# Optimization experiments

Measured on AMD Instinct MI355X. Metric: run time of the kernel, lower is better.

The kernel has to match this reference:

```python
import jax, jax.numpy as jnp
import numpy as np

H, KV, D, HID = 36, 4, 128, 4608   # heads, kv heads, head_dim, hidden
THETA = 100000.0
NEG = -1e30


def _rope_neox(pos, x):
    # pos: [T] int, x: [T, nh, D]; neox style: rotate half
    half = D // 2
    inv_freq = 1.0 / (THETA ** (jnp.arange(half, dtype=jnp.float32) / half))
    ang = pos.astype(jnp.float32)[:, None] * inv_freq          # [T, half]
    cos = jnp.cos(ang)[:, None, :]
    sin = jnp.sin(ang)[:, None, :]
    x1, x2 = x[..., :half], x[..., half:]
    return jnp.concatenate([x1 * cos - x2 * sin, x2 * cos + x1 * sin], axis=-1)


def setup_inputs() -> dict:
    key = jax.random.key(0)
    ks = jax.random.split(key, 6)
    T = 2048
    return {
        "positions": jnp.arange(T, dtype=jnp.int32),
        "hidden_states": jax.random.normal(ks[0], (T, HID), dtype=jnp.float32),
        "wqkv": jax.random.normal(ks[1], (H * D + 2 * KV * D, HID), dtype=jnp.float32) * 0.02,
        "bqkv": jax.random.normal(ks[2], (H * D + 2 * KV * D,), dtype=jnp.float32) * 0.02,
        "wo": jax.random.normal(ks[3], (HID, H * D), dtype=jnp.float32) * 0.02,
        "bo": jax.random.normal(ks[4], (HID,), dtype=jnp.float32) * 0.02,
        "window": 1024,
    }


def reference(positions, hidden_states, wqkv, bqkv, wo, bo, window):
    T = hidden_states.shape[0]
    qkv = hidden_states @ wqkv.T + bqkv                         # [T, 5632]
    q, k, v = jnp.split(qkv, [H * D, H * D + KV * D], axis=-1)
    q = q.reshape(T, H, D)
    k = k.reshape(T, KV, D)
    v = v.reshape(T, KV, D)
    q = _rope_neox(positions, q)
    k = _rope_neox(positions, k)
    # GQA: expand kv heads to query heads
    g = H // KV
    k = jnp.repeat(k, g, axis=1)                                # [T, H, D]
    v = jnp.repeat(v, g, axis=1)
    scale = D ** -0.5
    scores = jnp.einsum('thd,shd->hts', q, k) * scale           # [H, T, T]
    t = jnp.arange(T)
    # causal + sliding window: attend to s in (t - window, t]
    mask = (t[None, :] <= t[:, None]) & (t[None, :] > t[:, None] - window)
    scores = jnp.where(mask[None, :, :], scores, NEG)
    p = jax.nn.softmax(scores, axis=-1)
    attn = jnp.einsum('hts,shd->thd', p, v).reshape(T, H * D)
    return attn @ wo.T + bo
```

## Files before the change

kernel.cpp:

```cpp
#include <hip/hip_runtime.h>
#include <hip/hip_bf16.h>
#include <math.h>


#define T_SEQ   2048
#define HIDDEN  4608
#define NHEAD   36
#define NKVH    4
#define HEADDIM 128
#define GQA_G   9
#define NQKV    5632
#define KOFF    4608
#define VOFF    5120
#define BQ 64
#define BS 32
#define NTILE   64
#define PSTR 40

typedef short    bf16x8 __attribute__((ext_vector_type(8)));
typedef _Float16 f16x8  __attribute__((ext_vector_type(8)));
typedef _Float16 f16x4  __attribute__((ext_vector_type(4)));
typedef float    f32x4  __attribute__((ext_vector_type(4)));

__device__ inline bf16x8 pack8(float4 u, float4 v) {
    union { bf16x8 v8; __hip_bfloat162 h[4]; } r;
    r.h[0] = __float22bfloat162_rn(make_float2(u.x, u.y));
    r.h[1] = __float22bfloat162_rn(make_float2(u.z, u.w));
    r.h[2] = __float22bfloat162_rn(make_float2(v.x, v.y));
    r.h[3] = __float22bfloat162_rn(make_float2(v.z, v.w));
    return r.v8;
}

typedef const __attribute__((address_space(1))) int* gas_ptr;
typedef __attribute__((address_space(3))) int*       las_ptr;
__device__ __forceinline__ void gload_lds16(const void* g, void* l) {
    __builtin_amdgcn_global_load_lds((gas_ptr)g, (las_ptr)l, 16, 0, 0);
}

__global__ __launch_bounds__(256)
void cvt_bf16_kernel(const float* __restrict__ in, __hip_bfloat16* __restrict__ out,
                     int n8)
{
    for (int i = blockIdx.x * 256 + threadIdx.x; i < n8; i += gridDim.x * 256) {
        const float4 a = *(const float4*)(in + (size_t)i * 8);
        const float4 b = *(const float4*)(in + (size_t)i * 8 + 4);
        *(bf16x8*)(out + (size_t)i * 8) = pack8(a, b);
    }
}

template <typename OutT>
__global__ __launch_bounds__(256)
void gemm_bf16bt_kernel(const __hip_bfloat16* __restrict__ A,
                        const __hip_bfloat16* __restrict__ B,
                        const float* __restrict__ bias,
                        OutT* __restrict__ C, int N, int K)
{
    __shared__ short As[2][128 * 32];
    __shared__ short Bs[2][128 * 32];

    const int tid  = threadIdx.x;
    const int lane = tid & 63;
    const int wave = tid >> 6;

    const int nbx = gridDim.x;
    const int nwg = nbx * gridDim.y;
    int lin = blockIdx.y * nbx + blockIdx.x;
    lin = (lin & 7) * (nwg >> 3) + (lin >> 3);
    const int row0 = (lin / nbx) * 128;
    const int col0 = (lin % nbx) * 128;

    const int wr   = (wave >> 1) * 64;
    const int wc   = (wave & 1) * 64;
    const int fr   = lane & 15;
    const int fk   = (lane >> 4) * 8;

    const int srow = lane >> 2;
    const int scol = (lane & 3) * 8;

    const __hip_bfloat16* Ag0 = A + (size_t)(row0 + wave * 32 + srow) * K + scol;
    const __hip_bfloat16* Ag1 = Ag0 + (size_t)16 * K;
    const __hip_bfloat16* Bg0 = B + (size_t)(col0 + wave * 32 + srow) * K + scol;
    const __hip_bfloat16* Bg1 = Bg0 + (size_t)16 * K;

    short* Al0[2] = { &As[0][(wave * 32) * 32],      &As[1][(wave * 32) * 32] };
    short* Al1[2] = { &As[0][(wave * 32 + 16) * 32], &As[1][(wave * 32 + 16) * 32] };
    short* Bl0[2] = { &Bs[0][(wave * 32) * 32],      &Bs[1][(wave * 32) * 32] };
    short* Bl1[2] = { &Bs[0][(wave * 32 + 16) * 32], &Bs[1][(wave * 32 + 16) * 32] };

    f32x4 acc[4][4];
    #pragma unroll
    for (int i = 0; i < 4; ++i)
        #pragma unroll
        for (int j = 0; j < 4; ++j)
            #pragma unroll
            for (int r = 0; r < 4; ++r) acc[i][j][r] = 0.0f;

    gload_lds16(Ag0, Al0[0]);
    gload_lds16(Ag1, Al1[0]);
    gload_lds16(Bg0, Bl0[0]);
    gload_lds16(Bg1, Bl1[0]);
    __syncthreads();
    int cur = 0;

    for (int k0 = 0; k0 < K; k0 += 32) {
        if (k0 + 32 < K) {
            const int kn = k0 + 32;
            const int nb = cur ^ 1;
            gload_lds16(Ag0 + kn, Al0[nb]);
            gload_lds16(Ag1 + kn, Al1[nb]);
            gload_lds16(Bg0 + kn, Bl0[nb]);
            gload_lds16(Bg1 + kn, Bl1[nb]);
        }

        bf16x8 af[4], bfr[4];
        #pragma unroll
        for (int i = 0; i < 4; ++i)
            af[i] = *(const bf16x8*)&As[cur][(wr + i * 16 + fr) * 32 + fk];
        #pragma unroll
        for (int j = 0; j < 4; ++j)
            bfr[j] = *(const bf16x8*)&Bs[cur][(wc + j * 16 + fr) * 32 + fk];

        #pragma unroll
        for (int i = 0; i < 4; ++i)
            #pragma unroll
            for (int j = 0; j < 4; ++j)
                acc[i][j] = __builtin_amdgcn_mfma_f32_16x16x32_bf16(
                    af[i], bfr[j], acc[i][j], 0, 0, 0);

        __syncthreads();
        cur ^= 1;
    }

    const int quad = lane >> 4;
    #pragma unroll
    for (int j = 0; j < 4; ++j) {
        const int col = col0 + wc + j * 16 + fr;
        const float bv = bias[col];
        #pragma unroll
        for (int i = 0; i < 4; ++i) {
            const int rowb = row0 + wr + i * 16 + quad * 4;
            #pragma unroll
            for (int r = 0; r < 4; ++r)
                C[(size_t)(rowb + r) * N + col] = (OutT)(acc[i][j][r] + bv);
        }
    }
}

__global__ __launch_bounds__(256)
void prep_kv_kernel(const int* __restrict__ positions,
                    const _Float16* __restrict__ qkv,
                    _Float16* __restrict__ Kt,
                    _Float16* __restrict__ Vt)
{
    const int tile = blockIdx.x;
    const int kvh  = blockIdx.y;
    const int t    = threadIdx.x;
    const size_t ib = ((size_t)kvh * NTILE + tile) * 4096;

    {
        const int s   = t >> 3;
        const int j8  = (t & 7) * 8;
        const int row = tile * BS + s;
        const _Float16* kp = qkv + (size_t)row * NQKV + KOFF + kvh * HEADDIM;
        const f16x8 xa = *(const f16x8*)(kp + j8);
        const f16x8 xb = *(const f16x8*)(kp + 64 + j8);
        const float pos = (float)positions[row];
        f16x8 H1, H2;
        #pragma unroll
        for (int j = 0; j < 8; ++j) {
            const int d = j8 + j;
            const float inv_freq = __expf(-(float)d * (11.512925465f / 64.0f));
            float sn, cs;
            sincosf(pos * inv_freq, &sn, &cs);
            const float x1 = (float)xa[j];
            const float x2 = (float)xb[j];
            H1[j] = (_Float16)(x1 * cs - x2 * sn);
            H2[j] = (_Float16)(x2 * cs + x1 * sn);
        }
        const int gd1 = (t & 7);
        const int gd2 = gd1 + 8;
        *(f16x8*)&Kt[ib + gd1 * 256 + s * 8] = H1;
        *(f16x8*)&Kt[ib + gd2 * 256 + s * 8] = H2;
    }

    {
        const int q  = t >> 6;
        const int d0 = (t & 63) * 2;
        const _Float16* vp = qkv + (size_t)(tile * BS + q * 8) * NQKV + VOFF
                           + kvh * HEADDIM + d0;
        f16x8 V0, V1;
        #pragma unroll
        for (int j = 0; j < 8; ++j) {
            union { unsigned u; _Float16 h[2]; } w;
            w.u = *(const unsigned*)(vp + (size_t)j * NQKV);
            V0[j] = w.h[0];
            V1[j] = w.h[1];
        }
        *(f16x8*)&Vt[ib + q * 1024 + d0 * 8]       = V0;
        *(f16x8*)&Vt[ib + q * 1024 + (d0 + 1) * 8] = V1;
    }
}

__global__ __launch_bounds__(256)
void attn_kernel(const _Float16* __restrict__ qkv,
                 const int* __restrict__ positions,
                 const _Float16* __restrict__ Kt,
                 const _Float16* __restrict__ Vt,
                 __hip_bfloat16* __restrict__ out,
                 const int* __restrict__ windowp)
{
    __shared__ _Float16 KS[2][4096];
    __shared__ _Float16 VS[2][4096];
    __shared__ _Float16 Ps[4][16 * PSTR];

    const int h    = blockIdx.x;
    const int q0   = (T_SEQ / BQ - 1 - blockIdx.y) * BQ;
    const int kvh  = h / GQA_G;
    const int tid  = threadIdx.x;
    const int lane = tid & 63;
    const int wave = tid >> 6;
    const int l15  = lane & 15;
    const int quad = lane >> 4;
    const int window = *windowp;
    const float scale = 0.088388347648318447f * 1.4426950408889634f;

    f16x8 qf[4];
    const int q_g = q0 + wave * 16 + l15;
    {
        const _Float16* qp = qkv + (size_t)q_g * NQKV + h * HEADDIM + quad * 8;
        float qv[32];
        #pragma unroll
        for (int ks = 0; ks < 4; ++ks) {
            const f16x8 qa = *(const f16x8*)(qp + ks * 32);
            #pragma unroll
            for (int j = 0; j < 8; ++j) qv[ks * 8 + j] = (float)qa[j];
        }
        const float pos = (float)positions[q_g];
        #pragma unroll
        for (int p = 0; p < 2; ++p)
            #pragma unroll
            for (int j = 0; j < 8; ++j) {
                const int d = p * 32 + quad * 8 + j;
                const float inv_freq = __expf(-(float)d * (11.512925465f / 64.0f));
                float sn, cs;
                sincosf(pos * inv_freq, &sn, &cs);
                const float x1 = qv[p * 8 + j];
                const float x2 = qv[(p + 2) * 8 + j];
                qv[p * 8 + j]       = x1 * cs - x2 * sn;
                qv[(p + 2) * 8 + j] = x2 * cs + x1 * sn;
            }
        #pragma unroll
        for (int ks = 0; ks < 4; ++ks)
            #pragma unroll
            for (int j = 0; j < 8; ++j)
                qf[ks][j] = (_Float16)(qv[ks * 8 + j] * scale);
    }

    f32x4 o[8];
    #pragma unroll
    for (int c = 0; c < 8; ++c)
        #pragma unroll
        for (int r = 0; r < 4; ++r) o[c][r] = 0.0f;
    float mrun = -1e9f;
    float lrun = 0.0f;

    int s_lo = q0 - window + 1;
    if (s_lo < 0) s_lo = 0;
    s_lo &= ~(BS - 1);
    const int tile0  = s_lo >> 5;
    const int ntiles = ((q0 + BQ) - s_lo) >> 5;

    const _Float16* gK = Kt + ((size_t)kvh * NTILE) * 4096;
    const _Float16* gV = Vt + ((size_t)kvh * NTILE) * 4096;

    _Float16* Psw = &Ps[wave][0];

    auto STAGE = [&](int buf, int tile) {
        const size_t toff = (size_t)tile * 4096;
        #pragma unroll
        for (int i = 0; i < 2; ++i) {
            const int off = (wave * 2 + i) * 512;
            gload_lds16(gK + toff + off + lane * 8, &KS[buf][off]);
            gload_lds16(gV + toff + off + lane * 8, &VS[buf][off]);
        }
    };

    STAGE(0, tile0);
    __syncthreads();
    int cur = 0;

    for (int it = 0; it < ntiles; ++it) {
        const int st = s_lo + it * BS;
        if (it + 1 < ntiles) STAGE(cur ^ 1, tile0 + it + 1);

        f32x4 acc0, acc1;
        #pragma unroll
        for (int r = 0; r < 4; ++r) { acc0[r] = 0.0f; acc1[r] = 0.0f; }
        #pragma unroll
        for (int ks = 0; ks < 4; ++ks) {
            const int g = (ks * 4 + quad) * 256;
            const f16x8 b0 = *(const f16x8*)&KS[cur][g + l15 * 8];
            const f16x8 b1 = *(const f16x8*)&KS[cur][g + (16 + l15) * 8];
            acc0 = __builtin_amdgcn_mfma_f32_16x16x32_f16(b0, qf[ks], acc0, 0, 0, 0);
            acc1 = __builtin_amdgcn_mfma_f32_16x16x32_f16(b1, qf[ks], acc1, 0, 0, 0);
        }

        const int dq = q_g - st;
        float sv[8];
        #pragma unroll
        for (int r = 0; r < 4; ++r) {
            const int o0 = quad * 4 + r;
            const bool v0 = (unsigned)(dq - o0)      < (unsigned)window;
            const bool v1 = (unsigned)(dq - o0 - 16) < (unsigned)window;
            sv[r]     = v0 ? acc0[r] : -2e9f;
            sv[4 + r] = v1 ? acc1[r] : -2e9f;
        }
        float mx = sv[0];
        #pragma unroll
        for (int i = 1; i < 8; ++i) mx = fmaxf(mx, sv[i]);
        mx = fmaxf(mx, __shfl_xor(mx, 16));
        mx = fmaxf(mx, __shfl_xor(mx, 32));
        if (__any(mx > mrun + 8.0f)) {
            const float mnew  = fmaxf(mrun, mx);
            const float alpha = __builtin_amdgcn_exp2f(mrun - mnew);
            mrun = mnew;
            lrun *= alpha;
            #pragma unroll
            for (int c = 0; c < 8; ++c)
                #pragma unroll
                for (int r = 0; r < 4; ++r) o[c][r] *= alpha;
        }
        float e[8];
        float sum = 0.0f;
        #pragma unroll
        for (int i = 0; i < 8; ++i) {
            e[i] = __builtin_amdgcn_exp2f(sv[i] - mrun);
            sum += e[i];
        }
        sum += __shfl_xor(sum, 16);
        sum += __shfl_xor(sum, 32);
        lrun += sum;

        f16x4 pl, ph;
        #pragma unroll
        for (int r = 0; r < 4; ++r) { pl[r] = (_Float16)e[r]; ph[r] = (_Float16)e[4 + r]; }
        *(f16x4*)&Psw[l15 * PSTR + quad * 4]      = pl;
        *(f16x4*)&Psw[l15 * PSTR + 16 + quad * 4] = ph;
        const f16x8 pa = *(const f16x8*)&Psw[l15 * PSTR + quad * 8];

        #pragma unroll
        for (int c = 0; c < 8; ++c) {
            const f16x8 vb = *(const f16x8*)&VS[cur][quad * 1024 + (16 * c + l15) * 8];
            o[c] = __builtin_amdgcn_mfma_f32_16x16x32_f16(vb, pa, o[c], 0, 0, 0);
        }

        __syncthreads();
        cur ^= 1;
    }

    {
        const float inv = 1.0f / lrun;
        __hip_bfloat16* op = out + (size_t)q_g * (NHEAD * HEADDIM)
                           + h * HEADDIM + quad * 4;
        #pragma unroll
        for (int c = 0; c < 8; ++c) {
            union { ushort4 u; __hip_bfloat16 x[4]; } w;
            #pragma unroll
            for (int r = 0; r < 4; ++r) w.x[r] = __float2bfloat16(o[c][r] * inv);
            *(ushort4*)&op[16 * c] = w.u;
        }
    }
}

extern "C" void kernel_launch(void* const* d_in, const int* in_sizes, int n_in,
                              void* d_out, int out_size, void* d_ws, size_t ws_size,
                              hipStream_t stream)
{
    const int*   positions = (const int*)d_in[0];
    const float* hidden    = (const float*)d_in[1];
    const float* wqkv      = (const float*)d_in[2];
    const float* bqkv      = (const float*)d_in[3];
    const float* wo        = (const float*)d_in[4];
    const float* bo        = (const float*)d_in[5];
    const int*   windowp   = (const int*)d_in[6];
    float* outp = (float*)d_out;

    _Float16* qkv16 = (_Float16*)d_ws;
    __hip_bfloat16* hbf  = (__hip_bfloat16*)(qkv16 + (size_t)T_SEQ * NQKV);
    __hip_bfloat16* wqbf = hbf  + (size_t)T_SEQ * HIDDEN;
    __hip_bfloat16* wobf = wqbf + (size_t)NQKV * HIDDEN;
    __hip_bfloat16* abf  = wobf + (size_t)HIDDEN * HIDDEN;
    _Float16*       Kt   = (_Float16*)(abf + (size_t)T_SEQ * HIDDEN);
    _Float16*       Vt   = Kt + (size_t)NKVH * NTILE * 4096;

    cvt_bf16_kernel<<<1024, 256, 0, stream>>>(hidden, hbf, T_SEQ * HIDDEN / 8);
    cvt_bf16_kernel<<<2048, 256, 0, stream>>>(wqkv, wqbf, NQKV * HIDDEN / 8);
    cvt_bf16_kernel<<<2048, 256, 0, stream>>>(wo, wobf, HIDDEN * HIDDEN / 8);

    gemm_bf16bt_kernel<_Float16><<<dim3(NQKV / 128, T_SEQ / 128), 256, 0, stream>>>(
        hbf, wqbf, bqkv, qkv16, NQKV, HIDDEN);

    prep_kv_kernel<<<dim3(NTILE, NKVH), 256, 0, stream>>>(
        positions, qkv16, Kt, Vt);

    attn_kernel<<<dim3(NHEAD, T_SEQ / BQ), 256, 0, stream>>>(
        qkv16, positions, Kt, Vt, abf, windowp);

    gemm_bf16bt_kernel<float><<<dim3(HIDDEN / 128, T_SEQ / 128), 256, 0, stream>>>(
        abf, wobf, bo, outp, HIDDEN, HIDDEN);
}
```

Baseline: 579.9 us.

## Triple-buffer GEMM LDS loads with vmcnt waits and one barrier per step

The bf16 GEMM moves from a double-buffered to a triple-buffered LDS pipeline. It prefetches two K-tiles ahead and waits with explicit s_waitcnt vmcnt counts, so each iteration needs a single barrier instead of a full __syncthreads after the MFMAs. It also removes the grouped workgroup-index swizzle and maps blocks straight from blockIdx. This adds LDS usage, which may reduce occupancy, and dropping the swizzle may hurt L2 locality.

```diff
diff --git a/kernel.cpp b/kernel.cpp
--- a/kernel.cpp
+++ b/kernel.cpp
@@ -55,19 +55,14 @@
                         const float* __restrict__ bias,
                         OutT* __restrict__ C, int N, int K)
 {
-    __shared__ short As[2][128 * 32];
-    __shared__ short Bs[2][128 * 32];
+    __shared__ short As[3][128 * 32];
+    __shared__ short Bs[3][128 * 32];
 
     const int tid  = threadIdx.x;
     const int lane = tid & 63;
     const int wave = tid >> 6;
-
-    const int nbx = gridDim.x;
-    const int nwg = nbx * gridDim.y;
-    int lin = blockIdx.y * nbx + blockIdx.x;
-    lin = (lin & 7) * (nwg >> 3) + (lin >> 3);
-    const int row0 = (lin / nbx) * 128;
-    const int col0 = (lin % nbx) * 128;
+    const int row0 = blockIdx.y * 128;
+    const int col0 = blockIdx.x * 128;
 
     const int wr   = (wave >> 1) * 64;
     const int wc   = (wave & 1) * 64;
@@ -82,10 +77,10 @@
     const __hip_bfloat16* Bg0 = B + (size_t)(col0 + wave * 32 + srow) * K + scol;
     const __hip_bfloat16* Bg1 = Bg0 + (size_t)16 * K;
 
-    short* Al0[2] = { &As[0][(wave * 32) * 32],      &As[1][(wave * 32) * 32] };
-    short* Al1[2] = { &As[0][(wave * 32 + 16) * 32], &As[1][(wave * 32 + 16) * 32] };
-    short* Bl0[2] = { &Bs[0][(wave * 32) * 32],      &Bs[1][(wave * 32) * 32] };
-    short* Bl1[2] = { &Bs[0][(wave * 32 + 16) * 32], &Bs[1][(wave * 32 + 16) * 32] };
+    short* Al0[3] = { &As[0][(wave * 32) * 32],      &As[1][(wave * 32) * 32],      &As[2][(wave * 32) * 32] };
+    short* Al1[3] = { &As[0][(wave * 32 + 16) * 32], &As[1][(wave * 32 + 16) * 32], &As[2][(wave * 32 + 16) * 32] };
+    short* Bl0[3] = { &Bs[0][(wave * 32) * 32],      &Bs[1][(wave * 32) * 32],      &Bs[2][(wave * 32) * 32] };
+    short* Bl1[3] = { &Bs[0][(wave * 32 + 16) * 32], &Bs[1][(wave * 32 + 16) * 32], &Bs[2][(wave * 32 + 16) * 32] };
 
     f32x4 acc[4][4];
     #pragma unroll
@@ -94,18 +89,31 @@
         for (int j = 0; j < 4; ++j)
             #pragma unroll
             for (int r = 0; r < 4; ++r) acc[i][j][r] = 0.0f;
+
+    const int NK = K >> 5;
 
     gload_lds16(Ag0, Al0[0]);
     gload_lds16(Ag1, Al1[0]);
     gload_lds16(Bg0, Bl0[0]);
     gload_lds16(Bg1, Bl1[0]);
-    __syncthreads();
+    gload_lds16(Ag0 + 32, Al0[1]);
+    gload_lds16(Ag1 + 32, Al1[1]);
+    gload_lds16(Bg0 + 32, Bl0[1]);
+    gload_lds16(Bg1 + 32, Bl1[1]);
+
     int cur = 0;
-
-    for (int k0 = 0; k0 < K; k0 += 32) {
-        if (k0 + 32 < K) {
-            const int kn = k0 + 32;
-            const int nb = cur ^ 1;
+    for (int t = 0; t < NK; ++t) {
+        if (t + 1 < NK) {
+            asm volatile("s_waitcnt vmcnt(4)" ::: "memory");
+        } else {
+            asm volatile("s_waitcnt vmcnt(0)" ::: "memory");
+        }
+        __builtin_amdgcn_s_barrier();
+        __builtin_amdgcn_sched_barrier(0);
+
+        if (t + 2 < NK) {
+            const int kn = (t + 2) * 32;
+            int nb = cur + 2; if (nb >= 3) nb -= 3;
             gload_lds16(Ag0 + kn, Al0[nb]);
             gload_lds16(Ag1 + kn, Al1[nb]);
             gload_lds16(Bg0 + kn, Bl0[nb]);
@@ -127,8 +135,7 @@
                 acc[i][j] = __builtin_amdgcn_mfma_f32_16x16x32_bf16(
                     af[i], bfr[j], acc[i][j], 0, 0, 0);
 
-        __syncthreads();
-        cur ^= 1;
+        cur += 1; if (cur == 3) cur = 0;
     }
 
     const int quad = lane >> 4;
```

New measurement: 601.5 us. 1.04x slower.
